# Kernel optimization log

Hardware: AMD Instinct MI355X
Metric: run time of the kernel (lower is better)

Reference implementation:

```python
import jax, jax.numpy as jnp
import numpy as np
from jax import lax

B, C_IN, H, W = 16, 64, 64, 64
C_OUT, K, P, NC = 128, 3, 1, 512
PS = C_IN * K * K  # 576 patch feature size


def setup_inputs() -> dict:
    key = jax.random.key(0)
    k0, k1, k2, k3 = jax.random.split(key, 4)
    x = jax.random.normal(k0, (B, C_IN, H, W), jnp.float32)
    cluster_centers = jax.random.normal(k1, (NC, PS), jnp.float32)
    temp = jnp.ones((1,), jnp.float32)
    weight = jax.random.normal(k2, (C_OUT, C_IN, K, K), jnp.float32) * 0.05
    bias = jax.random.normal(k3, (C_OUT,), jnp.float32) * 0.05
    return {"x": x, "cluster_centers": cluster_centers, "temp": temp,
            "weight": weight, "bias": bias}


def _forward(x, cluster_centers, temp, weight, bias):
    Bx, C, Hx, Wx = x.shape
    t = temp.reshape(())  # scalar temperature
    # F.unfold: patches ordered (c, kh, kw) along feature dim -> [B, C*K*K, H, W]
    patches = lax.conv_general_dilated_patches(
        x, (K, K), (1, 1), padding=((P, P), (P, P)))
    L = Hx * Wx  # number of blocks; equals Wx*Wx (H==W, same-padding, stride 1)
    cols = patches.reshape(Bx, PS, L)               # this_patch
    flat = cols.transpose(0, 2, 1).reshape(-1, PS)  # [N, PS] flat_patches
    # torch.cdist (p=2): stable squared-distance expansion, single GEMM
    d2 = (jnp.sum(flat * flat, axis=1, keepdims=True)
          + jnp.sum(cluster_centers * cluster_centers, axis=1)[None, :]
          - 2.0 * (flat @ cluster_centers.T))
    dist = jnp.sqrt(jnp.maximum(d2, 0.0))           # [N, NC]
    soft = jax.nn.softmax(-dist * t, axis=1)        # soft assignments
    transformed = soft @ cluster_centers            # [N, PS]
    final = (t * transformed + flat) / (t + 1.0)
    # Faithful to the original's view_as: raw reshape WITHOUT transposing back
    final = final.reshape(Bx, PS, L)
    # F.fold(output_size=(W*K, W*K), kernel=K, padding=P, stride=K):
    # non-overlapping tiles on padded canvas, then crop P from each side.
    # (b, c, kh, kw, bh, bw) -> (b, c, bh, kh, bw, kw)
    tile = (final.reshape(Bx, C, K, K, Wx, Wx)
                 .transpose(0, 1, 4, 2, 5, 3)
                 .reshape(Bx, C, Wx * K, Wx * K))
    # crop offset P=1 at the top/left; bottom/right of cropped region is zero
    x_refold = jnp.pad(tile[:, :, P:, P:], ((0, 0), (0, 0), (0, P), (0, P)))
    # F.conv2d(..., stride=kernel_size, padding=padding)
    out = lax.conv_general_dilated(
        x_refold, weight, window_strides=(K, K), padding=((P, P), (P, P)),
        dimension_numbers=("NCHW", "OIHW", "NCHW"))
    return out + bias[None, :, None, None]


def reference(x, cluster_centers, temp, weight, bias):
    return _forward(x, cluster_centers, temp, weight, bias)
```

## Files before the change

### kernel.cpp

```cpp
#include <hip/hip_runtime.h>
#include <stdint.h>

typedef __bf16 bf16;
typedef bf16 bf16x2 __attribute__((ext_vector_type(2)));
typedef bf16 bf16x8 __attribute__((ext_vector_type(8)));
typedef float f32x4 __attribute__((ext_vector_type(4)));

static constexpr int B_    = 16;
static constexpr int C_IN  = 64;
static constexpr int H_    = 64;
static constexpr int W_    = 64;
static constexpr int C_OUT = 128;
static constexpr int NC    = 512;
static constexpr int PS    = 576;
static constexpr int L_    = H_ * W_;
static constexpr int NR    = B_ * L_;

#define DEVI __device__ __forceinline__

DEVI void gload_lds16(const void* g, void* l) {
  __builtin_amdgcn_global_load_lds(
      (const __attribute__((address_space(1))) uint32_t*)g,
      (__attribute__((address_space(3))) uint32_t*)l, 16, 0, 0);
}


__global__ void prep_w_kernel(const float* __restrict__ w, bf16* __restrict__ WB,
                              bf16* __restrict__ ccT) {
  int i = blockIdx.x * 256 + threadIdx.x;
  if (i < C_OUT * PS) WB[i] = (bf16)w[i];
  if (i < 64 * NC) ccT[(size_t)PS * NC + i] = (bf16)0.f;
}

__global__ void prep_cc_kernel(const float* __restrict__ cc, bf16* __restrict__ ccB,
                               bf16* __restrict__ ccT, float* __restrict__ cn) {
  int j = blockIdx.x;
  const float* src = cc + (size_t)j * PS;
  float s = 0.f;
  for (int p = threadIdx.x; p < PS; p += 256) {
    float v = src[p];
    bf16 bv = (bf16)v;
    ccB[(size_t)j * PS + p] = bv;
    ccT[(size_t)p * NC + j] = bv;
    float fv = (float)bv;
    s += fv * fv;
  }
  for (int o = 32; o; o >>= 1) s += __shfl_xor(s, o);
  __shared__ float red[4];
  int lane = threadIdx.x & 63, wid = threadIdx.x >> 6;
  if (lane == 0) red[wid] = s;
  __syncthreads();
  if (threadIdx.x == 0) cn[j] = red[0] + red[1] + red[2] + red[3];
}

static constexpr int XS_STRIDE = 66;
static constexpr int XS_PLANE  = 64 * XS_STRIDE;
static constexpr int XS_OFF    = 2;

__global__ void __launch_bounds__(256, 4) patch_kernel(
    const float* __restrict__ x, bf16* __restrict__ flatB,
    float* __restrict__ rn, float* __restrict__ rsum) {
  __shared__ bf16 xs[XS_OFF + 3 * XS_PLANE + 64];
  const int bh = blockIdx.x;
  const int b = bh >> 6, h = bh & 63;
  const size_t bOff = (size_t)b * (C_IN * L_);

#pragma unroll
  for (int it = 0; it < 12; ++it) {
    int idx = threadIdx.x + it * 256;
    int plane = idx >> 10;
    int rem = idx & 1023;
    int c = rem >> 4;
    int f4 = rem & 15;
    int y = h + plane - 1;
    int e = XS_OFF + plane * XS_PLANE + c * XS_STRIDE + f4 * 4;
    bf16x2 lo = {(bf16)0.f, (bf16)0.f}, hi = {(bf16)0.f, (bf16)0.f};
    if ((unsigned)y < 64u) {
      float4 v = *(const float4*)(x + bOff + (size_t)c * L_ + y * 64 + f4 * 4);
      lo = bf16x2{(bf16)v.x, (bf16)v.y};
      hi = bf16x2{(bf16)v.z, (bf16)v.w};
    }
    *(bf16x2*)(xs + e) = lo;
    *(bf16x2*)(xs + e + 2) = hi;
  }
  __syncthreads();

  const int lane = threadIdx.x & 63, wid = threadIdx.x >> 6;
  int eb[8], km[8];
#pragma unroll
  for (int q = 0; q < 8; q++) {
    int p = lane * 8 + q;
    int c = p / 9, r9 = p - c * 9;
    int kh = r9 / 3, kw = r9 - kh * 3;
    eb[q] = kh * XS_PLANE + c * XS_STRIDE + (kw - 1);
    km[q] = kw - 1;
  }
  int ebt[8], kmt[8];
  {
    int pl = (lane & 7) * 8;
#pragma unroll
    for (int q = 0; q < 8; q++) {
      int p = 512 + pl + q;
      int c = p / 9, r9 = p - c * 9;
      int kh = r9 / 3, kw = r9 - kh * 3;
      ebt[q] = kh * XS_PLANE + c * XS_STRIDE + (kw - 1);
      kmt[q] = kw - 1;
    }
  }

  for (int it = 0; it < 16; ++it) {
    int w = wid * 16 + it;
    int row = bh * 64 + w;
    bf16* outp = flatB + (size_t)row * PS;
    float s = 0.f;
    bf16x8 v;
#pragma unroll
    for (int q = 0; q < 8; q++) {
      int xx = w + km[q];
      float fv = ((unsigned)xx < 64u) ? (float)xs[XS_OFF + eb[q] + w] : 0.f;
      v[q] = (bf16)fv;
      s += fv * fv;
    }
    *(bf16x8*)(outp + lane * 8) = v;
    if (lane < 8) {
      bf16x8 v2;
#pragma unroll
      for (int q = 0; q < 8; q++) {
        int xx = w + kmt[q];
        float fv = ((unsigned)xx < 64u) ? (float)xs[XS_OFF + ebt[q] + w] : 0.f;
        v2[q] = (bf16)fv;
        s += fv * fv;
      }
      *(bf16x8*)(outp + 512 + lane * 8) = v2;
    }
    for (int o = 32; o; o >>= 1) s += __shfl_xor(s, o);
    if (lane == 0) { rn[row] = s; rsum[row] = 0.f; }
  }
}

__global__ void transpose_mask_kernel(const bf16* __restrict__ finalB, bf16* __restrict__ VT) {
  int b = blockIdx.z;
  int l0 = blockIdx.x * 64, p0 = blockIdx.y * 64;
  const bf16* src = finalB + (size_t)b * L_ * PS;
  bf16* dst = VT + (size_t)b * L_ * PS;
  __shared__ bf16 tile[64][72];
  for (int s = threadIdx.x; s < 512; s += 256) {
    int i = s >> 3, ch = s & 7;
    bf16x8 v = *(const bf16x8*)(src + (size_t)(p0 + i) * L_ + l0 + ch * 8);
#pragma unroll
    for (int q = 0; q < 8; q++) tile[ch * 8 + q][i] = v[q];
  }
  __syncthreads();
  for (int s = threadIdx.x; s < 512; s += 256) {
    int r = s >> 3, c = s & 7;
    int l = l0 + r;
    int oh = l >> 6, ow = l & 63;
    bf16x8 v;
#pragma unroll
    for (int q = 0; q < 8; q++) {
      int p = p0 + c * 8 + q;
      int r9 = p % 9;
      int kh = r9 / 3, kw = r9 - kh * 3;
      bf16 val = tile[r][c * 8 + q];
      if ((oh == 0 && kh == 0) || (ow == 0 && kw == 0)) val = (bf16)0.f;
      v[q] = val;
    }
    *(bf16x8*)(dst + (size_t)l * PS + p0 + c * 8) = v;
  }
}

template <int EPI, int GX = 0>
__global__ void __launch_bounds__(256, 4) gemm_nt(
    const bf16* __restrict__ A, int lda, const bf16* __restrict__ Bm, int ldb,
    int M, int N, int Kd,
    const float* __restrict__ e0, const float* __restrict__ e1,
    const float* __restrict__ e2, const bf16* flatB,
    float* outF, bf16* outB, int ldc) {
  int bx, by;
  if constexpr (GX > 0) {
    int b = blockIdx.x;
    int xcd = b & 7;
    int k = b >> 3;
    int ypx = (gridDim.x >> 3) / GX;
    bx = k % GX;
    by = xcd * ypx + k / GX;
  } else {
    bx = blockIdx.x;
    by = blockIdx.y;
  }
  if constexpr (EPI == 3) {
    size_t bz = blockIdx.z;
    Bm += bz * (size_t)L_ * PS;
    outF += bz * (size_t)C_OUT * L_;
  }
  __shared__ bf16 As[128 * 64];
  __shared__ bf16 Bs[128 * 64];
  const int tid = threadIdx.x;
  const int lane = tid & 63;
  const int wid = tid >> 6;
  const int wr = wid >> 1, wc = wid & 1;
  const int m0 = by * 128, n0 = bx * 128;

  const int srow = tid >> 3;
  const int sch = ((tid & 7) ^ (srow & 7)) * 8;
  const bf16* gA = A + (size_t)(m0 + srow) * lda + sch;
  const bf16* gB = Bm + (size_t)(n0 + srow) * ldb + sch;
  bf16* lA = As + tid * 8;
  bf16* lB = Bs + tid * 8;

  const int lrow = lane & 15;
  const int kq = lane >> 4;
  const int axor = lrow & 7;
  const int arow = (wr * 64 + lrow) * 64;
  const int brow = (wc * 64 + lrow) * 64;

  f32x4 acc[4][4];
#pragma unroll
  for (int i = 0; i < 4; i++)
#pragma unroll
    for (int j = 0; j < 4; j++) acc[i][j] = f32x4{0.f, 0.f, 0.f, 0.f};

  const int nk = Kd >> 6;
  for (int kt = 0; kt < nk; ++kt) {
    __syncthreads();
    const bf16* ga = gA + kt * 64;
    const bf16* gb = gB + kt * 64;
#pragma unroll
    for (int q = 0; q < 4; ++q) {
      gload_lds16(ga + (size_t)(q * 32) * lda, lA + q * 2048);
      gload_lds16(gb + (size_t)(q * 32) * ldb, lB + q * 2048);
    }
    __syncthreads();
#pragma unroll
    for (int h = 0; h < 2; ++h) {
      const int cs = ((h * 4 + kq) ^ axor) * 8;
      bf16x8 af[4], bfr[4];
#pragma unroll
      for (int i = 0; i < 4; i++) af[i] = *(const bf16x8*)(As + arow + i * 1024 + cs);
#pragma unroll
      for (int j = 0; j < 4; j++) bfr[j] = *(const bf16x8*)(Bs + brow + j * 1024 + cs);
#pragma unroll
      for (int i = 0; i < 4; i++)
#pragma unroll
        for (int j = 0; j < 4; j++)
          acc[i][j] = __builtin_amdgcn_mfma_f32_16x16x32_bf16(af[i], bfr[j], acc[i][j], 0, 0, 0);
    }
  }

  const int rb = m0 + wr * 64 + kq * 4;
  const int cb = n0 + wc * 64 + lrow;
  if constexpr (EPI == 1) {
    float t = e2[0];
#pragma unroll
    for (int i = 0; i < 4; i++) {
      float rowsum[4] = {0.f, 0.f, 0.f, 0.f};
#pragma unroll
      for (int j = 0; j < 4; j++) {
        int col = cb + j * 16;
        float cnv = e1[col];
#pragma unroll
        for (int r = 0; r < 4; r++) {
          int row = rb + i * 16 + r;
          float d2 = e0[row] + cnv - 2.f * acc[i][j][r];
          float e = __expf(-t * sqrtf(fmaxf(d2, 0.f)));
          outB[(size_t)row * ldc + col] = (bf16)e;
          rowsum[r] += e;
        }
      }
#pragma unroll
      for (int r = 0; r < 4; r++) {
        float s = rowsum[r];
        s += __shfl_xor(s, 1);
        s += __shfl_xor(s, 2);
        s += __shfl_xor(s, 4);
        s += __shfl_xor(s, 8);
        if (lrow == 0) atomicAdd(outF + rb + i * 16 + r, s);
      }
    }
  } else if constexpr (EPI == 2) {
    float t = e0[0];
    float inv = 1.f / (t + 1.f);
#pragma unroll
    for (int i = 0; i < 4; i++) {
      float arw[4];
#pragma unroll
      for (int r = 0; r < 4; r++) arw[r] = t * inv / e1[rb + i * 16 + r];
#pragma unroll
      for (int j = 0; j < 4; j++) {
        int col = cb + j * 16;
        if (col < N) {
#pragma unroll
          for (int r = 0; r < 4; r++) {
            int row = rb + i * 16 + r;
            float fl = (float)flatB[(size_t)row * PS + col];
            float v = acc[i][j][r] * arw[r] + fl * inv;
            outB[(size_t)row * ldc + col] = (bf16)v;
          }
        }
      }
    }
  } else {
#pragma unroll
    for (int i = 0; i < 4; i++) {
#pragma unroll
      for (int j = 0; j < 4; j++) {
        int col = cb + j * 16;
#pragma unroll
        for (int r = 0; r < 4; r++) {
          int row = rb + i * 16 + r;
          outF[(size_t)row * ldc + col] = acc[i][j][r] + e0[row];
        }
      }
    }
  }
}


extern "C" void kernel_launch(void* const* d_in, const int* in_sizes, int n_in,
                              void* d_out, int out_size, void* d_ws, size_t ws_size,
                              hipStream_t stream) {
  (void)in_sizes; (void)n_in; (void)out_size; (void)ws_size;
  const float* x    = (const float*)d_in[0];
  const float* cc   = (const float*)d_in[1];
  const float* tp   = (const float*)d_in[2];
  const float* w    = (const float*)d_in[3];
  const float* bias = (const float*)d_in[4];
  float* out = (float*)d_out;

  char* ws = (char*)d_ws;
  size_t off = 0;
  auto alloc = [&](size_t bytes) {
    char* p = ws + off;
    off += (bytes + 255) & ~(size_t)255;
    return p;
  };
  bf16* ccB   = (bf16*)alloc((size_t)NC * PS * 2);
  bf16* ccT   = (bf16*)alloc((size_t)640 * NC * 2);
  float* cn   = (float*)alloc((size_t)NC * 4);
  bf16* WB    = (bf16*)alloc((size_t)C_OUT * PS * 2);
  float* rn   = (float*)alloc((size_t)NR * 4);
  float* rsum = (float*)alloc((size_t)NR * 4);
  bf16* flatB = (bf16*)alloc((size_t)NR * PS * 2);
  char* Ereg  = alloc((size_t)NR * PS * 2);
  bf16* E  = (bf16*)Ereg;
  bf16* VT = (bf16*)Ereg;

  prep_w_kernel<<<dim3(288), dim3(256), 0, stream>>>(w, WB, ccT);
  prep_cc_kernel<<<dim3(NC), dim3(256), 0, stream>>>(cc, ccB, ccT, cn);
  patch_kernel<<<dim3(B_ * H_), dim3(256), 0, stream>>>(x, flatB, rn, rsum);
  gemm_nt<1, 4><<<dim3((NC / 128) * (NR / 128)), dim3(256), 0, stream>>>(
      flatB, PS, ccB, PS, NR, NC, PS, rn, cn, tp, nullptr, rsum, E, NC);
  gemm_nt<2, 5><<<dim3(5 * (NR / 128)), dim3(256), 0, stream>>>(
      E, NC, ccT, NC, NR, PS, NC, tp, rsum, nullptr, flatB, nullptr, flatB, PS);
  transpose_mask_kernel<<<dim3(64, 9, B_), dim3(256), 0, stream>>>(flatB, VT);
  gemm_nt<3><<<dim3(L_ / 128, 1, B_), dim3(256), 0, stream>>>(
      WB, PS, VT, PS, C_OUT, L_, PS, bias, nullptr, nullptr, nullptr, out, nullptr, L_);
}
```

Measured before the change: 250.3 us.

## Use 256x256 double-buffered 512-thread GEMM tiles for the two cluster GEMMs

```diff
diff --git a/kernel.cpp b/kernel.cpp
--- a/kernel.cpp
+++ b/kernel.cpp
@@ -29,7 +29,7 @@
                               bf16* __restrict__ ccT) {
   int i = blockIdx.x * 256 + threadIdx.x;
   if (i < C_OUT * PS) WB[i] = (bf16)w[i];
-  if (i < 64 * NC) ccT[(size_t)PS * NC + i] = (bf16)0.f;
+  if (i < 192 * NC) ccT[(size_t)PS * NC + i] = (bf16)0.f;
 }
 
 __global__ void prep_cc_kernel(const float* __restrict__ cc, bf16* __restrict__ ccB,
@@ -64,7 +64,6 @@
   const int bh = blockIdx.x;
   const int b = bh >> 6, h = bh & 63;
   const size_t bOff = (size_t)b * (C_IN * L_);
-
 #pragma unroll
   for (int it = 0; it < 12; ++it) {
     int idx = threadIdx.x + it * 256;
@@ -107,7 +106,6 @@
       kmt[q] = kw - 1;
     }
   }
-
   for (int it = 0; it < 16; ++it) {
     int w = wid * 16 + it;
     int row = bh * 64 + w;
@@ -169,90 +167,107 @@
   }
 }
 
-template <int EPI, int GX = 0>
-__global__ void __launch_bounds__(256, 4) gemm_nt(
+template <int EPI, int GX>
+__global__ void __launch_bounds__(512, 2) gemm_big256(
     const bf16* __restrict__ A, int lda, const bf16* __restrict__ Bm, int ldb,
     int M, int N, int Kd,
     const float* __restrict__ e0, const float* __restrict__ e1,
     const float* __restrict__ e2, const bf16* flatB,
     float* outF, bf16* outB, int ldc) {
-  int bx, by;
-  if constexpr (GX > 0) {
-    int b = blockIdx.x;
-    int xcd = b & 7;
-    int k = b >> 3;
-    int ypx = (gridDim.x >> 3) / GX;
-    bx = k % GX;
-    by = xcd * ypx + k / GX;
-  } else {
-    bx = blockIdx.x;
-    by = blockIdx.y;
-  }
-  if constexpr (EPI == 3) {
-    size_t bz = blockIdx.z;
-    Bm += bz * (size_t)L_ * PS;
-    outF += bz * (size_t)C_OUT * L_;
-  }
-  __shared__ bf16 As[128 * 64];
-  __shared__ bf16 Bs[128 * 64];
+  const int blk = blockIdx.x;
+  const int xcd = blk & 7;
+  const int kk = blk >> 3;
+  const int ypx = (gridDim.x >> 3) / GX;
+  const int bx = kk % GX;
+  const int by = xcd * ypx + kk / GX;
+  const int m0 = by * 256, n0 = bx * 256;
+
+  __shared__ bf16 As[2][256 * 64];
+  __shared__ bf16 Bs[2][256 * 64];
+
   const int tid = threadIdx.x;
   const int lane = tid & 63;
   const int wid = tid >> 6;
-  const int wr = wid >> 1, wc = wid & 1;
-  const int m0 = by * 128, n0 = bx * 128;
+  const int wr = wid >> 2;
+  const int wc = wid & 3;
+  const int lrow = lane & 15;
+  const int kq = lane >> 4;
 
   const int srow = tid >> 3;
   const int sch = ((tid & 7) ^ (srow & 7)) * 8;
   const bf16* gA = A + (size_t)(m0 + srow) * lda + sch;
   const bf16* gB = Bm + (size_t)(n0 + srow) * ldb + sch;
-  bf16* lA = As + tid * 8;
-  bf16* lB = Bs + tid * 8;
-
-  const int lrow = lane & 15;
-  const int kq = lane >> 4;
+  const int dst = tid * 8;
+
   const int axor = lrow & 7;
-  const int arow = (wr * 64 + lrow) * 64;
+  const int arow = (wr * 128 + lrow) * 64;
   const int brow = (wc * 64 + lrow) * 64;
 
-  f32x4 acc[4][4];
-#pragma unroll
-  for (int i = 0; i < 4; i++)
+  f32x4 acc[8][4];
+#pragma unroll
+  for (int i = 0; i < 8; i++)
 #pragma unroll
     for (int j = 0; j < 4; j++) acc[i][j] = f32x4{0.f, 0.f, 0.f, 0.f};
 
+  auto stageA = [&](int kt, int bi) {
+    const bf16* a0 = gA + kt * 64;
+#pragma unroll
+    for (int q = 0; q < 4; ++q)
+      gload_lds16(a0 + (size_t)(q * 64) * lda, &As[bi][q * 4096 + dst]);
+  };
+  auto stageB = [&](int kt, int bi) {
+    const bf16* b0 = gB + kt * 64;
+#pragma unroll
+    for (int q = 0; q < 4; ++q)
+      gload_lds16(b0 + (size_t)(q * 64) * ldb, &Bs[bi][q * 4096 + dst]);
+  };
+
   const int nk = Kd >> 6;
+  stageA(0, 0);
+  stageB(0, 0);
   for (int kt = 0; kt < nk; ++kt) {
-    __syncthreads();
-    const bf16* ga = gA + kt * 64;
-    const bf16* gb = gB + kt * 64;
-#pragma unroll
-    for (int q = 0; q < 4; ++q) {
-      gload_lds16(ga + (size_t)(q * 32) * lda, lA + q * 2048);
-      gload_lds16(gb + (size_t)(q * 32) * ldb, lB + q * 2048);
-    }
-    __syncthreads();
-#pragma unroll
-    for (int h = 0; h < 2; ++h) {
-      const int cs = ((h * 4 + kq) ^ axor) * 8;
-      bf16x8 af[4], bfr[4];
-#pragma unroll
-      for (int i = 0; i < 4; i++) af[i] = *(const bf16x8*)(As + arow + i * 1024 + cs);
-#pragma unroll
-      for (int j = 0; j < 4; j++) bfr[j] = *(const bf16x8*)(Bs + brow + j * 1024 + cs);
-#pragma unroll
-      for (int i = 0; i < 4; i++)
-#pragma unroll
-        for (int j = 0; j < 4; j++)
-          acc[i][j] = __builtin_amdgcn_mfma_f32_16x16x32_bf16(af[i], bfr[j], acc[i][j], 0, 0, 0);
-    }
-  }
-
-  const int rb = m0 + wr * 64 + kq * 4;
+    const int cur = kt & 1;
+    if (kt + 1 < nk) {
+      stageA(kt + 1, cur ^ 1);
+      asm volatile("s_waitcnt vmcnt(4)" ::: "memory");
+    } else {
+      asm volatile("s_waitcnt vmcnt(0)" ::: "memory");
+    }
+    __builtin_amdgcn_s_barrier();
+    __builtin_amdgcn_sched_barrier(0);
+    if (kt + 1 < nk) stageB(kt + 1, cur ^ 1);
+
+    const bf16* Ab = As[cur];
+    const bf16* Bb = Bs[cur];
+    bf16x8 bfr[4][2];
+#pragma unroll
+    for (int j = 0; j < 4; j++)
+#pragma unroll
+      for (int kh = 0; kh < 2; kh++)
+        bfr[j][kh] = *(const bf16x8*)(Bb + brow + j * 1024 + (((kh * 4 + kq) ^ axor) * 8));
+    __builtin_amdgcn_s_setprio(1);
+#pragma unroll
+    for (int i = 0; i < 8; i++) {
+      bf16x8 a0 = *(const bf16x8*)(Ab + arow + i * 1024 + (((0 * 4 + kq) ^ axor) * 8));
+      bf16x8 a1 = *(const bf16x8*)(Ab + arow + i * 1024 + (((1 * 4 + kq) ^ axor) * 8));
+#pragma unroll
+      for (int j = 0; j < 4; j++)
+        acc[i][j] = __builtin_amdgcn_mfma_f32_16x16x32_bf16(a0, bfr[j][0], acc[i][j], 0, 0, 0);
+#pragma unroll
+      for (int j = 0; j < 4; j++)
+        acc[i][j] = __builtin_amdgcn_mfma_f32_16x16x32_bf16(a1, bfr[j][1], acc[i][j], 0, 0, 0);
+    }
+    __builtin_amdgcn_s_setprio(0);
+    __builtin_amdgcn_sched_barrier(0);
+    __builtin_amdgcn_s_barrier();
+  }
+
+  const int rb = m0 + wr * 128 + kq * 4;
   const int cb = n0 + wc * 64 + lrow;
   if constexpr (EPI == 1) {
     float t = e2[0];
 #pragma unroll
-    for (int i = 0; i < 4; i++) {
+    for (int i = 0; i < 8; i++) {
       float rowsum[4] = {0.f, 0.f, 0.f, 0.f};
 #pragma unroll
       for (int j = 0; j < 4; j++) {
@@ -277,11 +292,11 @@
         if (lrow == 0) atomicAdd(outF + rb + i * 16 + r, s);
       }
     }
-  } else if constexpr (EPI == 2) {
+  } else {
     float t = e0[0];
     float inv = 1.f / (t + 1.f);
 #pragma unroll
-    for (int i = 0; i < 4; i++) {
+    for (int i = 0; i < 8; i++) {
       float arw[4];
 #pragma unroll
       for (int r = 0; r < 4; r++) arw[r] = t * inv / e1[rb + i * 16 + r];
@@ -299,17 +314,80 @@
         }
       }
     }
-  } else {
-#pragma unroll
-    for (int i = 0; i < 4; i++) {
-#pragma unroll
-      for (int j = 0; j < 4; j++) {
-        int col = cb + j * 16;
-#pragma unroll
-        for (int r = 0; r < 4; r++) {
-          int row = rb + i * 16 + r;
-          outF[(size_t)row * ldc + col] = acc[i][j][r] + e0[row];
-        }
+  }
+}
+
+__global__ void __launch_bounds__(256, 4) gemm3_kernel(
+    const bf16* __restrict__ A, int lda, const bf16* __restrict__ Bm, int ldb,
+    int Kd, const float* __restrict__ bias, float* outF, int ldc) {
+  size_t bz = blockIdx.z;
+  Bm += bz * (size_t)L_ * PS;
+  outF += bz * (size_t)C_OUT * L_;
+  __shared__ bf16 As[128 * 64];
+  __shared__ bf16 Bs[128 * 64];
+  const int tid = threadIdx.x;
+  const int lane = tid & 63;
+  const int wid = tid >> 6;
+  const int wr = wid >> 1, wc = wid & 1;
+  const int n0 = blockIdx.x * 128;
+
+  const int srow = tid >> 3;
+  const int sch = ((tid & 7) ^ (srow & 7)) * 8;
+  const bf16* gA = A + (size_t)srow * lda + sch;
+  const bf16* gB = Bm + (size_t)(n0 + srow) * ldb + sch;
+  bf16* lA = As + tid * 8;
+  bf16* lB = Bs + tid * 8;
+
+  const int lrow = lane & 15;
+  const int kq = lane >> 4;
+  const int axor = lrow & 7;
+  const int arow = (wr * 64 + lrow) * 64;
+  const int brow = (wc * 64 + lrow) * 64;
+
+  f32x4 acc[4][4];
+#pragma unroll
+  for (int i = 0; i < 4; i++)
+#pragma unroll
+    for (int j = 0; j < 4; j++) acc[i][j] = f32x4{0.f, 0.f, 0.f, 0.f};
+
+  const int nk = Kd >> 6;
+  for (int kt = 0; kt < nk; ++kt) {
+    __syncthreads();
+    const bf16* ga = gA + kt * 64;
+    const bf16* gb = gB + kt * 64;
+#pragma unroll
+    for (int q = 0; q < 4; ++q) {
+      gload_lds16(ga + (size_t)(q * 32) * lda, lA + q * 2048);
+      gload_lds16(gb + (size_t)(q * 32) * ldb, lB + q * 2048);
+    }
+    __syncthreads();
+#pragma unroll
+    for (int h = 0; h < 2; ++h) {
+      const int cs = ((h * 4 + kq) ^ axor) * 8;
+      bf16x8 af[4], bfr[4];
+#pragma unroll
+      for (int i = 0; i < 4; i++) af[i] = *(const bf16x8*)(As + arow + i * 1024 + cs);
+#pragma unroll
+      for (int j = 0; j < 4; j++) bfr[j] = *(const bf16x8*)(Bs + brow + j * 1024 + cs);
+#pragma unroll
+      for (int i = 0; i < 4; i++)
+#pragma unroll
+        for (int j = 0; j < 4; j++)
+          acc[i][j] = __builtin_amdgcn_mfma_f32_16x16x32_bf16(af[i], bfr[j], acc[i][j], 0, 0, 0);
+    }
+  }
+
+  const int rb = wr * 64 + kq * 4;
+  const int cb = n0 + wc * 64 + lrow;
+#pragma unroll
+  for (int i = 0; i < 4; i++) {
+#pragma unroll
+    for (int j = 0; j < 4; j++) {
+      int col = cb + j * 16;
+#pragma unroll
+      for (int r = 0; r < 4; r++) {
+        int row = rb + i * 16 + r;
+        outF[(size_t)row * ldc + col] = acc[i][j][r] + bias[row];
       }
     }
   }
@@ -335,7 +413,7 @@
     return p;
   };
   bf16* ccB   = (bf16*)alloc((size_t)NC * PS * 2);
-  bf16* ccT   = (bf16*)alloc((size_t)640 * NC * 2);
+  bf16* ccT   = (bf16*)alloc((size_t)768 * NC * 2);
   float* cn   = (float*)alloc((size_t)NC * 4);
   bf16* WB    = (bf16*)alloc((size_t)C_OUT * PS * 2);
   float* rn   = (float*)alloc((size_t)NR * 4);
@@ -345,14 +423,14 @@
   bf16* E  = (bf16*)Ereg;
   bf16* VT = (bf16*)Ereg;
 
-  prep_w_kernel<<<dim3(288), dim3(256), 0, stream>>>(w, WB, ccT);
+  prep_w_kernel<<<dim3(384), dim3(256), 0, stream>>>(w, WB, ccT);
   prep_cc_kernel<<<dim3(NC), dim3(256), 0, stream>>>(cc, ccB, ccT, cn);
   patch_kernel<<<dim3(B_ * H_), dim3(256), 0, stream>>>(x, flatB, rn, rsum);
-  gemm_nt<1, 4><<<dim3((NC / 128) * (NR / 128)), dim3(256), 0, stream>>>(
+  gemm_big256<1, 2><<<dim3((NR / 256) * 2), dim3(512), 0, stream>>>(
       flatB, PS, ccB, PS, NR, NC, PS, rn, cn, tp, nullptr, rsum, E, NC);
-  gemm_nt<2, 5><<<dim3(5 * (NR / 128)), dim3(256), 0, stream>>>(
+  gemm_big256<2, 3><<<dim3((NR / 256) * 3), dim3(512), 0, stream>>>(
       E, NC, ccT, NC, NR, PS, NC, tp, rsum, nullptr, flatB, nullptr, flatB, PS);
   transpose_mask_kernel<<<dim3(64, 9, B_), dim3(256), 0, stream>>>(flatB, VT);
-  gemm_nt<3><<<dim3(L_ / 128, 1, B_), dim3(256), 0, stream>>>(
-      WB, PS, VT, PS, C_OUT, L_, PS, bias, nullptr, nullptr, nullptr, out, nullptr, L_);
-}
+  gemm3_kernel<<<dim3(L_ / 128, 1, B_), dim3(256), 0, stream>>>(
+      WB, PS, VT, PS, PS, bias, out, L_);
+}
```

Result: slower. 304.6 us (+21.7%).
